# Optimization experiments

Measured on AMD Instinct MI355X. Metric: run time of the kernel, lower is better.

Reference implementation:

```python
import jax, jax.numpy as jnp
import numpy as np

V, E, H, T = 32000, 1024, 1024, 2048

def setup_inputs() -> dict:
    key = jax.random.key(0)
    ks = jax.random.split(key, 10)
    s = lambda k, shape: jax.random.normal(k, shape, dtype=jnp.float32) * 0.02
    return {
        "sequence": jax.random.randint(ks[0], (T,), 0, V),
        "h0": s(ks[1], (1, 1, H)),
        "c0": s(ks[2], (1, 1, H)),
        "emb": s(ks[3], (V, E)),
        "W_ih": s(ks[4], (4 * H, E)),
        "W_hh": s(ks[5], (4 * H, H)),
        "b_ih": s(ks[6], (4 * H,)),
        "b_hh": s(ks[7], (4 * H,)),
        "W_out": s(ks[8], (V, H)),
        "b_out": s(ks[9], (V,)),
    }

def reference(sequence, h0, c0, emb, W_ih, W_hh, b_ih, b_hh, W_out, b_out):
    x = emb[sequence]                      # [T, E] embedding lookup
    # Precompute input-to-gate projections for all timesteps (one big GEMM).
    xg = x @ W_ih.T + (b_ih + b_hh)        # [T, 4H]
    Hd = h0.shape[-1]

    def step(carry, xg_t):
        h, c = carry                       # [H], [H]
        gates = xg_t + h @ W_hh.T          # [4H], PyTorch packed order i,f,g,o
        i = jax.nn.sigmoid(gates[:Hd])
        f = jax.nn.sigmoid(gates[Hd:2 * Hd])
        g = jnp.tanh(gates[2 * Hd:3 * Hd])
        o = jax.nn.sigmoid(gates[3 * Hd:])
        c = f * c + i * g
        h = o * jnp.tanh(c)
        return (h, c), h

    (hT, cT), hs = jax.lax.scan(step, (h0[0, 0], c0[0, 0]), xg)  # hs: [T, H]
    scores = hs @ W_out.T + b_out          # [T, V]
    logp = jax.nn.log_softmax(scores, axis=-1)
    return logp, hT[None, None, :], cT[None, None, :]
```

## Files before the change

kernel.cpp:

```cpp
#include <hip/hip_runtime.h>


typedef __attribute__((ext_vector_type(8))) short short8;
typedef __attribute__((ext_vector_type(4))) float f32x4;
typedef __attribute__((ext_vector_type(4))) int i32x4;
typedef __attribute__((ext_vector_type(4))) unsigned short u16x4;

__device__ __forceinline__ float bf2f(unsigned short u) {
    unsigned int x = ((unsigned int)u) << 16;
    return __builtin_bit_cast(float, x);
}
__device__ __forceinline__ unsigned short f2bf(float f) {
    unsigned int x = __builtin_bit_cast(unsigned int, f);
    x += 0x7FFFu + ((x >> 16) & 1u);
    return (unsigned short)(x >> 16);
}

__global__ __launch_bounds__(256) void cast_f2b(
    const float* __restrict__ src, unsigned short* __restrict__ dst, int n4)
{
    int i = blockIdx.x * 256 + threadIdx.x;
    if (i < n4) {
        f32x4 v = ((const f32x4*)src)[i];
        u16x4 o;
        o.x = f2bf(v.x); o.y = f2bf(v.y); o.z = f2bf(v.z); o.w = f2bf(v.w);
        ((u16x4*)dst)[i] = o;
    }
}

__global__ __launch_bounds__(256) void gather_cast(
    const int* __restrict__ seq, const float* __restrict__ emb,
    unsigned short* __restrict__ xbf)
{
    int t = blockIdx.x, i = threadIdx.x;
    const f32x4* src = (const f32x4*)(emb + (size_t)seq[t] * 1024);
    f32x4 v = src[i];
    u16x4 o;
    o.x = f2bf(v.x); o.y = f2bf(v.y); o.z = f2bf(v.z); o.w = f2bf(v.w);
    ((u16x4*)(xbf + (size_t)t * 1024))[i] = o;
}

__global__ void init_h(const float* __restrict__ h0, float* __restrict__ hbuf)
{
    int i = blockIdx.x * 256 + threadIdx.x;
    if (i < 1024) hbuf[i] = h0[i];
}

__global__ __launch_bounds__(256) void gemm_bt(
    const unsigned short* __restrict__ A, const unsigned short* __restrict__ B,
    const float* __restrict__ bias0, const float* __restrict__ bias1,
    float* __restrict__ C, int K, int ldc)
{
    __shared__ __align__(16) unsigned short As[64 * 40];
    __shared__ __align__(16) unsigned short Bs[64 * 40];

    const int tid = threadIdx.x;
    const int m0 = blockIdx.y << 6, n0 = blockIdx.x << 6;
    const int wave = tid >> 6, lane = tid & 63, q = lane >> 4, l = lane & 15;

    f32x4 acc[4];
#pragma unroll
    for (int j = 0; j < 4; j++) acc[j] = (f32x4){0.f, 0.f, 0.f, 0.f};

    const int arow = tid >> 2;
    const int ach  = (tid & 3) * 8;

    for (int k0 = 0; k0 < K; k0 += 32) {
        __syncthreads();
        i32x4 av = *(const i32x4*)(A + (size_t)(m0 + arow) * K + k0 + ach);
        i32x4 bv = *(const i32x4*)(B + (size_t)(n0 + arow) * K + k0 + ach);
        *(i32x4*)(&As[arow * 40 + ach]) = av;
        *(i32x4*)(&Bs[arow * 40 + ach]) = bv;
        __syncthreads();
        short8 a = *(const short8*)(&As[(wave * 16 + l) * 40 + q * 8]);
#pragma unroll
        for (int j = 0; j < 4; j++) {
            short8 b = *(const short8*)(&Bs[(j * 16 + l) * 40 + q * 8]);
            acc[j] = __builtin_amdgcn_mfma_f32_16x16x32_bf16(a, b, acc[j], 0, 0, 0);
        }
    }

#pragma unroll
    for (int j = 0; j < 4; j++) {
        int col = n0 + j * 16 + l;
        float bias = 0.f;
        if (bias0) bias += bias0[col];
        if (bias1) bias += bias1[col];
        int row0 = m0 + wave * 16 + q * 4;
#pragma unroll
        for (int r = 0; r < 4; r++)
            C[(size_t)(row0 + r) * ldc + col] = acc[j][r] + bias;
    }
}

#define NWG 128
#define FSTRIDE 32
__global__ __launch_bounds__(256, 1) void lstm_scan(
    const float* __restrict__ Whh, const float* __restrict__ xg,
    const float* __restrict__ c0, float* __restrict__ hbuf,
    unsigned short* __restrict__ hs, int* __restrict__ flags,
    float* __restrict__ outHT, float* __restrict__ outCT, int T)
{
    __shared__ float lh[1024];
    const int tid = threadIdx.x, blk = blockIdx.x;
    const int u = tid >> 5, s = tid & 31;
    const int j = blk * 8 + u;

    float w[4][32];
#pragma unroll
    for (int g = 0; g < 4; g++) {
        const float* wr = Whh + (size_t)(g * 1024 + j) * 1024 + s * 32;
#pragma unroll
        for (int k = 0; k < 32; k++) w[g][k] = wr[(k + s) & 31];
    }

    const bool owner = (s == 0);
    float cst = owner ? c0[j] : 0.f;

    for (int t = 0; t < T; t++) {
        float xgi = 0.f, xgf = 0.f, xgg = 0.f, xgo = 0.f;
        if (owner) {
            const float* xp = xg + (size_t)t * 4096 + j;
            xgi = xp[0]; xgf = xp[1024]; xgg = xp[2048]; xgo = xp[3072];
        }

        if (t > 0) {
            if (tid < 64) {
                const int* fa = flags + tid * FSTRIDE;
                const int* fb = flags + (tid + 64) * FSTRIDE;
                for (;;) {
                    int f1 = __hip_atomic_load(fa, __ATOMIC_RELAXED,
                                               __HIP_MEMORY_SCOPE_AGENT);
                    int f2 = __hip_atomic_load(fb, __ATOMIC_RELAXED,
                                               __HIP_MEMORY_SCOPE_AGENT);
                    if (__all(f1 >= t && f2 >= t)) break;
                }
            }
            __syncthreads();
        }

        {
            const float* hb = hbuf + (t & 1) * 1024;
#pragma unroll
            for (int k2 = 0; k2 < 4; k2++) {
                float v = __hip_atomic_load(hb + tid + 256 * k2, __ATOMIC_RELAXED,
                                            __HIP_MEMORY_SCOPE_AGENT);
                lh[tid + 256 * k2] = v;
            }
        }
        __syncthreads();

        float a0 = 0.f, a1 = 0.f, a2 = 0.f, a3 = 0.f;
        const int base = s * 32;
#pragma unroll
        for (int k = 0; k < 32; k++) {
            float hk = lh[base + ((k + s) & 31)];
            a0 += w[0][k] * hk; a1 += w[1][k] * hk;
            a2 += w[2][k] * hk; a3 += w[3][k] * hk;
        }
#pragma unroll
        for (int d = 16; d; d >>= 1) {
            a0 += __shfl_down(a0, d, 32); a1 += __shfl_down(a1, d, 32);
            a2 += __shfl_down(a2, d, 32); a3 += __shfl_down(a3, d, 32);
        }

        float hv = 0.f;
        if (owner) {
            float gi = xgi + a0, gf = xgf + a1, gg = xgg + a2, go = xgo + a3;
            float iv = 1.f / (1.f + __expf(-gi));
            float fv = 1.f / (1.f + __expf(-gf));
            float gv = tanhf(gg);
            float ov = 1.f / (1.f + __expf(-go));
            cst = fv * cst + iv * gv;
            hv = ov * tanhf(cst);
            __hip_atomic_store(&hbuf[((t + 1) & 1) * 1024 + j], hv,
                               __ATOMIC_RELAXED, __HIP_MEMORY_SCOPE_AGENT);
            if (t == T - 1) { outHT[j] = hv; outCT[j] = cst; }
        }
        asm volatile("s_waitcnt vmcnt(0)" ::: "memory");
        __syncthreads();
        if (tid == 0)
            __hip_atomic_store(&flags[blk * FSTRIDE], t + 1, __ATOMIC_RELAXED,
                               __HIP_MEMORY_SCOPE_AGENT);
        if (owner) hs[(size_t)t * 1024 + j] = f2bf(hv);
    }
}

__global__ __launch_bounds__(256) void logsoftmax_rows(float* __restrict__ out, int V)
{
    __shared__ float redm[4], reds[4];
    const int tid = threadIdx.x;
    float* base = out + (size_t)blockIdx.x * V;
    const int n4 = V >> 2;

    float m = -3.0e38f, ssum = 0.f;
    for (int i = tid; i < n4; i += 256) {
        f32x4 v = ((const f32x4*)base)[i];
#pragma unroll
        for (int jj = 0; jj < 4; jj++) {
            float x = v[jj];
            if (x > m) { ssum = ssum * __expf(m - x) + 1.f; m = x; }
            else       { ssum += __expf(x - m); }
        }
    }
#pragma unroll
    for (int d = 32; d; d >>= 1) {
        float om = __shfl_down(m, d, 64);
        float os = __shfl_down(ssum, d, 64);
        float M = fmaxf(m, om);
        ssum = ssum * __expf(m - M) + os * __expf(om - M);
        m = M;
    }
    if ((tid & 63) == 0) { redm[tid >> 6] = m; reds[tid >> 6] = ssum; }
    __syncthreads();
    float M = fmaxf(fmaxf(redm[0], redm[1]), fmaxf(redm[2], redm[3]));
    float S = reds[0] * __expf(redm[0] - M) + reds[1] * __expf(redm[1] - M) +
              reds[2] * __expf(redm[2] - M) + reds[3] * __expf(redm[3] - M);
    float lse = M + logf(S);
    for (int i = tid; i < n4; i += 256) {
        f32x4 v = ((const f32x4*)base)[i];
        v.x -= lse; v.y -= lse; v.z -= lse; v.w -= lse;
        ((f32x4*)base)[i] = v;
    }
}

extern "C" void kernel_launch(void* const* d_in, const int* in_sizes, int n_in,
                              void* d_out, int out_size, void* d_ws, size_t ws_size,
                              hipStream_t stream)
{
    const int*   seq   = (const int*)d_in[0];
    const float* h0    = (const float*)d_in[1];
    const float* c0    = (const float*)d_in[2];
    const float* emb   = (const float*)d_in[3];
    const float* W_ih  = (const float*)d_in[4];
    const float* W_hh  = (const float*)d_in[5];
    const float* b_ih  = (const float*)d_in[6];
    const float* b_hh  = (const float*)d_in[7];
    const float* W_out = (const float*)d_in[8];
    const float* b_out = (const float*)d_in[9];

    const int T = 2048, H = 1024, V = 32000, G4 = 4096;

    char* ws = (char*)d_ws;
    float*          xg     = (float*)ws;
    unsigned short* Woutb  = (unsigned short*)(ws + 33554432);
    unsigned short* Wihb   = (unsigned short*)(ws + 99090432);
    unsigned short* xbf    = (unsigned short*)(ws + 107479040);
    unsigned short* hs     = (unsigned short*)(ws + 111673344);
    float*          hbuf   = (float*)(ws + 115867648);
    int*            flags  = (int*)(ws + 115875840);

    float* outp  = (float*)d_out;
    float* outHT = outp + (size_t)T * V;
    float* outCT = outHT + H;

    hipMemsetAsync(flags, 0, NWG * FSTRIDE * sizeof(int), stream);
    init_h<<<4, 256, 0, stream>>>(h0, hbuf);
    cast_f2b<<<(G4 * 1024 / 4 + 255) / 256, 256, 0, stream>>>(W_ih, Wihb, G4 * 1024 / 4);
    cast_f2b<<<(V * 1024 / 4 + 255) / 256, 256, 0, stream>>>(W_out, Woutb, V * 1024 / 4);
    gather_cast<<<T, 256, 0, stream>>>(seq, emb, xbf);

    gemm_bt<<<dim3(G4 / 64, T / 64), 256, 0, stream>>>(
        xbf, Wihb, b_ih, b_hh, xg, 1024, G4);

    lstm_scan<<<NWG, 256, 0, stream>>>(W_hh, xg, c0, hbuf, hs, flags, outHT, outCT, T);

    gemm_bt<<<dim3(V / 64, T / 64), 256, 0, stream>>>(
        hs, Woutb, b_out, nullptr, outp, 1024, V);

    logsoftmax_rows<<<T, 256, 0, stream>>>(outp, V);
}
```

Measured before the change: 8.311 ms.

## Replace per-block flag barrier with step-tagged hidden-state values

Each hidden value is now stored as a 64-bit word with the timestep in its upper half. Consumers spin directly on the values they need instead of first polling 128 per-block flags and then reading the hidden buffer. This removes the flag store, the extra waitcnt and __syncthreads, and one round trip per step on the serial scan's critical path. In exchange it adds double-buffered shared memory and heavier 64-bit polling traffic. Correctness relies on 64-bit atomic stores being single-copy atomic and on the double buffer not being overwritten early.

```diff
diff --git a/kernel.cpp b/kernel.cpp
--- a/kernel.cpp
+++ b/kernel.cpp
@@ -40,10 +40,14 @@
     ((u16x4*)(xbf + (size_t)t * 1024))[i] = o;
 }
 
-__global__ void init_h(const float* __restrict__ h0, float* __restrict__ hbuf)
+__global__ void init_h(const float* __restrict__ h0,
+                       unsigned long long* __restrict__ hpair)
 {
     int i = blockIdx.x * 256 + threadIdx.x;
-    if (i < 1024) hbuf[i] = h0[i];
+    if (i < 1024) {
+        hpair[i] = (unsigned long long)__builtin_bit_cast(unsigned int, h0[i]);
+        hpair[1024 + i] = 0xFFFFFFFF00000000ull;
+    }
 }
 
 __global__ __launch_bounds__(256) void gemm_bt(
@@ -94,14 +98,13 @@
 }
 
 #define NWG 128
-#define FSTRIDE 32
 __global__ __launch_bounds__(256, 1) void lstm_scan(
     const float* __restrict__ Whh, const float* __restrict__ xg,
-    const float* __restrict__ c0, float* __restrict__ hbuf,
-    unsigned short* __restrict__ hs, int* __restrict__ flags,
+    const float* __restrict__ c0, unsigned long long* __restrict__ hpair,
+    unsigned short* __restrict__ hs,
     float* __restrict__ outHT, float* __restrict__ outCT, int T)
 {
-    __shared__ float lh[1024];
+    __shared__ float lh[2][1024];
     const int tid = threadIdx.x, blk = blockIdx.x;
     const int u = tid >> 5, s = tid & 31;
     const int j = blk * 8 + u;
@@ -124,37 +127,52 @@
             xgi = xp[0]; xgf = xp[1024]; xgg = xp[2048]; xgo = xp[3072];
         }
 
-        if (t > 0) {
-            if (tid < 64) {
-                const int* fa = flags + tid * FSTRIDE;
-                const int* fb = flags + (tid + 64) * FSTRIDE;
-                for (;;) {
-                    int f1 = __hip_atomic_load(fa, __ATOMIC_RELAXED,
-                                               __HIP_MEMORY_SCOPE_AGENT);
-                    int f2 = __hip_atomic_load(fb, __ATOMIC_RELAXED,
-                                               __HIP_MEMORY_SCOPE_AGENT);
-                    if (__all(f1 >= t && f2 >= t)) break;
-                }
-            }
-            __syncthreads();
-        }
-
         {
-            const float* hb = hbuf + (t & 1) * 1024;
-#pragma unroll
-            for (int k2 = 0; k2 < 4; k2++) {
-                float v = __hip_atomic_load(hb + tid + 256 * k2, __ATOMIC_RELAXED,
-                                            __HIP_MEMORY_SCOPE_AGENT);
-                lh[tid + 256 * k2] = v;
-            }
+            const unsigned long long* hb = hpair + (size_t)(t & 1) * 1024;
+            const unsigned int want = (unsigned int)t;
+            bool g0 = false, g1 = false, g2 = false, g3 = false;
+            do {
+                if (!g0) {
+                    unsigned long long v = __hip_atomic_load(
+                        hb + tid, __ATOMIC_RELAXED, __HIP_MEMORY_SCOPE_AGENT);
+                    if ((unsigned int)(v >> 32) == want) {
+                        lh[t & 1][tid] = __builtin_bit_cast(float, (unsigned int)v);
+                        g0 = true;
+                    }
+                }
+                if (!g1) {
+                    unsigned long long v = __hip_atomic_load(
+                        hb + tid + 256, __ATOMIC_RELAXED, __HIP_MEMORY_SCOPE_AGENT);
+                    if ((unsigned int)(v >> 32) == want) {
+                        lh[t & 1][tid + 256] = __builtin_bit_cast(float, (unsigned int)v);
+                        g1 = true;
+                    }
+                }
+                if (!g2) {
+                    unsigned long long v = __hip_atomic_load(
+                        hb + tid + 512, __ATOMIC_RELAXED, __HIP_MEMORY_SCOPE_AGENT);
+                    if ((unsigned int)(v >> 32) == want) {
+                        lh[t & 1][tid + 512] = __builtin_bit_cast(float, (unsigned int)v);
+                        g2 = true;
+                    }
+                }
+                if (!g3) {
+                    unsigned long long v = __hip_atomic_load(
+                        hb + tid + 768, __ATOMIC_RELAXED, __HIP_MEMORY_SCOPE_AGENT);
+                    if ((unsigned int)(v >> 32) == want) {
+                        lh[t & 1][tid + 768] = __builtin_bit_cast(float, (unsigned int)v);
+                        g3 = true;
+                    }
+                }
+            } while (!(g0 && g1 && g2 && g3));
         }
         __syncthreads();
 
         float a0 = 0.f, a1 = 0.f, a2 = 0.f, a3 = 0.f;
-        const int base = s * 32;
+        const float* lhp = &lh[t & 1][s * 32];
 #pragma unroll
         for (int k = 0; k < 32; k++) {
-            float hk = lh[base + ((k + s) & 31)];
+            float hk = lhp[(k + s) & 31];
             a0 += w[0][k] * hk; a1 += w[1][k] * hk;
             a2 += w[2][k] * hk; a3 += w[3][k] * hk;
         }
@@ -164,7 +182,6 @@
             a2 += __shfl_down(a2, d, 32); a3 += __shfl_down(a3, d, 32);
         }
 
-        float hv = 0.f;
         if (owner) {
             float gi = xgi + a0, gf = xgf + a1, gg = xgg + a2, go = xgo + a3;
             float iv = 1.f / (1.f + __expf(-gi));
@@ -172,17 +189,15 @@
             float gv = tanhf(gg);
             float ov = 1.f / (1.f + __expf(-go));
             cst = fv * cst + iv * gv;
-            hv = ov * tanhf(cst);
-            __hip_atomic_store(&hbuf[((t + 1) & 1) * 1024 + j], hv,
+            float hv = ov * tanhf(cst);
+            unsigned long long pv =
+                ((unsigned long long)(unsigned int)(t + 1) << 32) |
+                (unsigned long long)__builtin_bit_cast(unsigned int, hv);
+            __hip_atomic_store(&hpair[(size_t)((t + 1) & 1) * 1024 + j], pv,
                                __ATOMIC_RELAXED, __HIP_MEMORY_SCOPE_AGENT);
+            hs[(size_t)t * 1024 + j] = f2bf(hv);
             if (t == T - 1) { outHT[j] = hv; outCT[j] = cst; }
         }
-        asm volatile("s_waitcnt vmcnt(0)" ::: "memory");
-        __syncthreads();
-        if (tid == 0)
-            __hip_atomic_store(&flags[blk * FSTRIDE], t + 1, __ATOMIC_RELAXED,
-                               __HIP_MEMORY_SCOPE_AGENT);
-        if (owner) hs[(size_t)t * 1024 + j] = f2bf(hv);
     }
 }
 
@@ -247,15 +262,13 @@
     unsigned short* Wihb   = (unsigned short*)(ws + 99090432);
     unsigned short* xbf    = (unsigned short*)(ws + 107479040);
     unsigned short* hs     = (unsigned short*)(ws + 111673344);
-    float*          hbuf   = (float*)(ws + 115867648);
-    int*            flags  = (int*)(ws + 115875840);
+    unsigned long long* hpair = (unsigned long long*)(ws + 115867648);
 
     float* outp  = (float*)d_out;
     float* outHT = outp + (size_t)T * V;
     float* outCT = outHT + H;
 
-    hipMemsetAsync(flags, 0, NWG * FSTRIDE * sizeof(int), stream);
-    init_h<<<4, 256, 0, stream>>>(h0, hbuf);
+    init_h<<<4, 256, 0, stream>>>(h0, hpair);
     cast_f2b<<<(G4 * 1024 / 4 + 255) / 256, 256, 0, stream>>>(W_ih, Wihb, G4 * 1024 / 4);
     cast_f2b<<<(V * 1024 / 4 + 255) / 256, 256, 0, stream>>>(W_out, Woutb, V * 1024 / 4);
     gather_cast<<<T, 256, 0, stream>>>(seq, emb, xbf);
@@ -263,7 +276,7 @@
     gemm_bt<<<dim3(G4 / 64, T / 64), 256, 0, stream>>>(
         xbf, Wihb, b_ih, b_hh, xg, 1024, G4);
 
-    lstm_scan<<<NWG, 256, 0, stream>>>(W_hh, xg, c0, hbuf, hs, flags, outHT, outCT, T);
+    lstm_scan<<<NWG, 256, 0, stream>>>(W_hh, xg, c0, hpair, hs, outHT, outCT, T);
 
     gemm_bt<<<dim3(V / 64, T / 64), 256, 0, stream>>>(
         hs, Woutb, b_out, nullptr, outp, 1024, V);
```

New measurement: 6.827 ms. -17.9%, faster.
